# Optimization experiments

Hardware: AMD Instinct MI355X
Metric: run time of the kernel (lower is better)

Reference implementation:

```python
import jax, jax.numpy as jnp
import numpy as np

D_MODEL = 1024
N_HEADS = 16
D_HEAD = D_MODEL // N_HEADS


def setup_inputs() -> dict:
    key = jax.random.key(0)
    ks = jax.random.split(key, 16)
    B, S, D = 2, 2048, D_MODEL
    s = 1.0 / np.sqrt(D)
    inp = {
        "query": jax.random.normal(ks[0], (B, S, D), jnp.float32),
        "key": jax.random.normal(ks[1], (B, S, D), jnp.float32),
        "value": jax.random.normal(ks[2], (B, S, D), jnp.float32),
        "pos_embedding": jax.random.normal(ks[3], (B, S, D), jnp.float32),
        "Wq": jax.random.normal(ks[4], (D, D), jnp.float32) * s,
        "bq": jnp.zeros((D,), jnp.float32),
        "Wk": jax.random.normal(ks[5], (D, D), jnp.float32) * s,
        "bk": jnp.zeros((D,), jnp.float32),
        "Wv": jax.random.normal(ks[6], (D, D), jnp.float32) * s,
        "bv": jnp.zeros((D,), jnp.float32),
        "Wpos": jax.random.normal(ks[7], (D, D), jnp.float32) * s,
        "u_bias": jax.random.normal(ks[8], (N_HEADS, D_HEAD), jnp.float32) * s,
        "v_bias": jax.random.normal(ks[9], (N_HEADS, D_HEAD), jnp.float32) * s,
        "Wout": jax.random.normal(ks[10], (D, D), jnp.float32) * s,
        "bout": jnp.zeros((D,), jnp.float32),
    }
    return inp


def _rel_shift(pos_score):
    # Transformer-XL relative shift: pad one zero column, reshape, drop first row.
    B, H, S1, S2 = pos_score.shape
    zeros = jnp.zeros((B, H, S1, 1), pos_score.dtype)
    padded = jnp.concatenate([zeros, pos_score], axis=-1)  # [B,H,S1,S2+1]
    padded = padded.reshape(B, H, S2 + 1, S1)
    return padded[:, :, 1:].reshape(B, H, S1, S2)


def reference(query, key, value, pos_embedding, Wq, bq, Wk, bk, Wv, bv, Wpos, u_bias, v_bias, Wout, bout):
    B, S, D = query.shape
    H, dh = N_HEADS, D_HEAD
    q = (query @ Wq + bq).reshape(B, S, H, dh)            # [B,S,H,dh]
    k = (key @ Wk + bk).reshape(B, S, H, dh)              # [B,S,H,dh]
    v = (value @ Wv + bv).reshape(B, S, H, dh)            # [B,S,H,dh]
    p = (pos_embedding @ Wpos).reshape(B, S, H, dh)       # [B,S,H,dh]

    content_score = jnp.einsum('bqhd,bkhd->bhqk', q + u_bias, k)
    pos_score = jnp.einsum('bqhd,bkhd->bhqk', q + v_bias, p)
    pos_score = _rel_shift(pos_score)

    score = (content_score + pos_score) / jnp.asarray(np.sqrt(D), score_dtype := content_score.dtype)
    attn = jax.nn.softmax(score, axis=-1)                 # [B,H,S,S]
    context = jnp.einsum('bhqk,bkhd->bqhd', attn, v).reshape(B, S, D)
    out = context @ Wout + bout
    return out, attn
```

## Files before the change

### kernel.cpp

```cpp
#include <hip/hip_runtime.h>

#define S_LEN 2048
#define DM    1024
#define NH    16
#define DH    64
#define BATCH 2
#define S2    ((size_t)S_LEN * S_LEN)

typedef _Float16 half_t;
typedef _Float16 f16x8 __attribute__((ext_vector_type(8)));
typedef _Float16 f16x4 __attribute__((ext_vector_type(4)));
typedef float    f32x4 __attribute__((ext_vector_type(4)));

__device__ __forceinline__ void gll16(const void* g, void* l) {
  __builtin_amdgcn_global_load_lds(
      (const __attribute__((address_space(1))) void*)g,
      (__attribute__((address_space(3))) void*)l, 16, 0, 0);
}

__device__ __forceinline__ void stage_gll(half_t* lds, const half_t* src, int stride) {
  const int t = threadIdx.x, w = t >> 6, lane = t & 63;
  const int c1 = lane & 7, r8 = lane >> 3;
#pragma unroll
  for (int it = 0; it < 4; ++it) {
    int r = w * 32 + it * 8 + r8;
    const half_t* g = src + (size_t)r * stride + ((c1 ^ r8) << 3);
    gll16(g, lds + (size_t)w * 2048 + it * 512);
  }
}

__device__ __forceinline__ void mfma_block(const half_t* At, const half_t* Bt,
                                           int w, int lane, f32x4 acc[2][8]) {
  const int grp = lane >> 4, li = lane & 15;
#pragma unroll
  for (int ks = 0; ks < 2; ++ks) {
    const int chunk = ks * 4 + grp;
    f16x8 a[2], b[8];
#pragma unroll
    for (int fr = 0; fr < 2; ++fr) {
      int r = w * 32 + fr * 16 + li;
      a[fr] = *(const f16x8*)&At[(size_t)(r * 8 + (chunk ^ (r & 7))) * 8];
    }
#pragma unroll
    for (int fc = 0; fc < 8; ++fc) {
      int r = fc * 16 + li;
      b[fc] = *(const f16x8*)&Bt[(size_t)(r * 8 + (chunk ^ (r & 7))) * 8];
    }
#pragma unroll
    for (int fr = 0; fr < 2; ++fr)
#pragma unroll
      for (int fc = 0; fc < 8; ++fc)
        acc[fr][fc] = __builtin_amdgcn_mfma_f32_16x16x32_f16(a[fr], b[fc], acc[fr][fc], 0, 0, 0);
  }
}

template<typename ST>
__device__ __forceinline__ void load8s(const ST* p, float* o) {
  if constexpr (sizeof(ST) == 2) {
    f16x8 v = *(const f16x8*)p;
#pragma unroll
    for (int e = 0; e < 8; ++e) o[e] = (float)v[e];
  } else {
    const float4* q = (const float4*)p;
    float4 a = q[0], b = q[1];
    o[0]=a.x; o[1]=a.y; o[2]=a.z; o[3]=a.w; o[4]=b.x; o[5]=b.y; o[6]=b.z; o[7]=b.w;
  }
}

struct AArgs { const float* src[4]; half_t* dst[4]; };

__global__ __launch_bounds__(256) void a2h(AArgs a, half_t* zbuf) {
  if (blockIdx.x == 0 && blockIdx.y == 0 && threadIdx.x < 8) {
    float4 z = {0.f, 0.f, 0.f, 0.f};
    ((float4*)zbuf)[threadIdx.x] = z;
  }
  const float* s = a.src[blockIdx.y];
  half_t* d = a.dst[blockIdx.y];
  size_t i = ((size_t)blockIdx.x * 256 + threadIdx.x) * 8;
  float4 v0 = *(const float4*)(s + i), v1 = *(const float4*)(s + i + 4);
  f16x8 h;
  h[0]=(half_t)v0.x; h[1]=(half_t)v0.y; h[2]=(half_t)v0.z; h[3]=(half_t)v0.w;
  h[4]=(half_t)v1.x; h[5]=(half_t)v1.y; h[6]=(half_t)v1.z; h[7]=(half_t)v1.w;
  *(f16x8*)(d + i) = h;
}

struct WArgs { const float* src[5]; half_t* dst[5]; };

__global__ __launch_bounds__(256) void wconv(WArgs wa) {
  __shared__ float T[64][65];
  const float* W = wa.src[blockIdx.z];
  half_t* D = wa.dst[blockIdx.z];
  const int k0 = blockIdx.x * 64, n0 = blockIdx.y * 64;
  const int t = threadIdx.x;
#pragma unroll
  for (int it = 0; it < 4; ++it) {
    int idx = t + it * 256; int r = idx >> 4, c4 = (idx & 15) * 4;
    float4 v = *(const float4*)(W + (size_t)(k0 + r) * DM + n0 + c4);
    T[r][c4] = v.x; T[r][c4 + 1] = v.y; T[r][c4 + 2] = v.z; T[r][c4 + 3] = v.w;
  }
  __syncthreads();
#pragma unroll
  for (int it = 0; it < 2; ++it) {
    int idx = t + it * 256; int n = idx >> 3, kc = (idx & 7) * 8;
    f16x8 o;
#pragma unroll
    for (int e = 0; e < 8; ++e) o[e] = (half_t)T[kc + e][n];
    *(f16x8*)&D[(size_t)(n0 + n) * DM + k0 + kc] = o;
  }
}

struct GArgs {
  const half_t* A[4];  const half_t* Bt[4];
  const float* ba[4]; const float* bu[4]; const float* bv[4];
  half_t* oa[4]; half_t* ob[4]; float* of[4];
};

template<bool F32OUT>
__global__ __launch_bounds__(256) void gemm_k(GArgs g, int K) {
  __shared__ __align__(16) half_t At[2][128 * 64];
  __shared__ __align__(16) half_t Bt[2][128 * 64];
  const int z = blockIdx.z;
  const half_t* A = g.A[z];
  const half_t* B = g.Bt[z];
  const int n0 = blockIdx.x * 128, m0 = blockIdx.y * 128;
  const int t = threadIdx.x, w = t >> 6, lane = t & 63;
  const f32x4 zf = {0.f, 0.f, 0.f, 0.f};
  f32x4 acc[2][8];
#pragma unroll
  for (int i = 0; i < 2; ++i)
#pragma unroll
    for (int j = 0; j < 8; ++j) acc[i][j] = zf;

  stage_gll(At[0], A + (size_t)m0 * K, K);
  stage_gll(Bt[0], B + (size_t)n0 * K, K);
  __syncthreads();
  int cur = 0;
  for (int k0 = 0; k0 < K; k0 += 64) {
    int nk = k0 + 64;
    if (nk < K) {
      stage_gll(At[cur ^ 1], A + (size_t)m0 * K + nk, K);
      stage_gll(Bt[cur ^ 1], B + (size_t)n0 * K + nk, K);
    }
    mfma_block(At[cur], Bt[cur], w, lane, acc);
    __syncthreads();
    cur ^= 1;
  }
  const int grp = lane >> 4, li = lane & 15;
#pragma unroll
  for (int fr = 0; fr < 2; ++fr)
#pragma unroll
    for (int fc = 0; fc < 8; ++fc)
#pragma unroll
      for (int r = 0; r < 4; ++r) {
        int row = m0 + w * 32 + fr * 16 + grp * 4 + r;
        int col = n0 + fc * 16 + li;
        float v = acc[fr][fc][r];
        if (g.ba[z]) v += g.ba[z][col];
        if constexpr (F32OUT) {
          g.of[z][(size_t)row * DM + col] = v;
        } else {
          float v1 = v + (g.bu[z] ? g.bu[z][col] : 0.f);
          g.oa[z][(size_t)row * DM + col] = (half_t)v1;
          if (g.ob[z]) g.ob[z][(size_t)row * DM + col] = (half_t)(v + g.bv[z][col]);
        }
      }
}

__global__ __launch_bounds__(256) void vtrans(const half_t* vp, half_t* vT) {
  __shared__ half_t T[64][72];
  const int s0 = blockIdx.x * 64, h = blockIdx.y, b = blockIdx.z;
  const int t = threadIdx.x;
#pragma unroll
  for (int it = 0; it < 2; ++it) {
    int idx = t + it * 256; int s = idx >> 3, c = idx & 7;
    uint4 v = *(const uint4*)(vp + ((size_t)(b * S_LEN + s0 + s)) * DM + h * DH + c * 8);
    *(uint4*)&T[s][c * 8] = v;
  }
  __syncthreads();
  half_t* dst = vT + ((size_t)(b * NH + h)) * DH * S_LEN;
#pragma unroll
  for (int it = 0; it < 2; ++it) {
    int idx = t + it * 256; int d = idx >> 3, sc = (idx & 7) * 8;
    f16x8 o;
#pragma unroll
    for (int e = 0; e < 8; ++e) o[e] = T[sc + e][d];
    *(f16x8*)&dst[(size_t)d * S_LEN + s0 + sc] = o;
  }
}

template<typename ST>
__global__ __launch_bounds__(512) void score_fused(
    const half_t* __restrict__ qu_, const half_t* __restrict__ qv_,
    const half_t* __restrict__ kp_, const half_t* __restrict__ pp_,
    const half_t* __restrict__ zbuf, ST* __restrict__ sc, float* __restrict__ part)
{
  __shared__ __align__(16) half_t Mf[36864];
  __shared__ __align__(16) half_t QV[144 * 64];
  __shared__ __align__(16) half_t Pb[256 * 64];
  half_t* QU = Mf;
  half_t* Kt = Mf + 8192;

  const int bh = blockIdx.z, b = bh >> 4, h = bh & 15;
  const int kt = blockIdx.x, qt = blockIdx.y;
  const int i0 = qt * 128, k0 = kt * 128;
  const int base = 1920 + k0 - i0;
  const int t = threadIdx.x, w = t >> 6, lane = t & 63;
  const int grp = lane >> 4, li = lane & 15;

  {
    const half_t* srcA = qu_ + ((size_t)(b * S_LEN + i0)) * DM + h * DH;
    const half_t* srcB = kp_ + ((size_t)(b * S_LEN + k0)) * DM + h * DH;
#pragma unroll
    for (int p = 0; p < 2; ++p) {
      int cidx = t + p * 512; int r = cidx >> 3, c = cidx & 7;
      gll16(srcA + (size_t)r * DM + ((c ^ (r & 7)) << 3), QU + (size_t)cidx * 8);
      gll16(srcB + (size_t)r * DM + ((c ^ (r & 7)) << 3), Kt + (size_t)cidx * 8);
    }
  }
#pragma unroll
  for (int p = 0; p < 3; ++p) {
    int cidx = t + p * 512;
    if (cidx < 1152) {
      int r = cidx >> 3, c = cidx & 7;
      int grow = i0 + r; if (grow > S_LEN - 1) grow = S_LEN - 1;
      gll16(qv_ + ((size_t)(b * S_LEN + grow)) * DM + h * DH + ((c ^ (r & 7)) << 3),
            QV + (size_t)cidx * 8);
    }
  }
#pragma unroll
  for (int p = 0; p < 4; ++p) {
    int cidx = t + p * 512; int e = cidx >> 3, c = cidx & 7;
    int jv = base + e; if (jv >= S_LEN + 1) jv -= (S_LEN + 1);
    const half_t* src = (jv == S_LEN)
        ? (zbuf + ((c ^ (e & 7)) << 3))
        : (pp_ + ((size_t)(b * S_LEN + jv)) * DM + h * DH + ((c ^ (e & 7)) << 3));
    gll16(src, Pb + (size_t)cidx * 8);
  }
  __syncthreads();

  const f32x4 zf = {0.f, 0.f, 0.f, 0.f};
  f32x4 acc_c[8];
#pragma unroll
  for (int j = 0; j < 8; ++j) acc_c[j] = zf;
#pragma unroll
  for (int kk = 0; kk < 2; ++kk) {
    const int chunk = kk * 4 + grp;
    int ra = w * 16 + li;
    f16x8 a = *(const f16x8*)&QU[(size_t)(ra * 8 + (chunk ^ (ra & 7))) * 8];
#pragma unroll
    for (int fc = 0; fc < 8; ++fc) {
      int rb = fc * 16 + li;
      f16x8 bf = *(const f16x8*)&Kt[(size_t)(rb * 8 + (chunk ^ (rb & 7))) * 8];
      acc_c[fc] = __builtin_amdgcn_mfma_f32_16x16x32_f16(a, bf, acc_c[fc], 0, 0, 0);
    }
  }
  __syncthreads();

  f16x8 bm[2][2];
#pragma unroll
  for (int kk = 0; kk < 2; ++kk)
#pragma unroll
    for (int eci = 0; eci < 2; ++eci) {
      int rb = (w + eci * 8) * 16 + li;
      bm[kk][eci] = *(const f16x8*)&Pb[(size_t)(rb * 8 + ((kk * 4 + grp) ^ (rb & 7))) * 8];
    }
  for (int rf = 0; rf < 9; ++rf) {
    f32x4 am[2] = {zf, zf};
#pragma unroll
    for (int kk = 0; kk < 2; ++kk) {
      int ra = rf * 16 + li;
      f16x8 a = *(const f16x8*)&QV[(size_t)(ra * 8 + ((kk * 4 + grp) ^ (ra & 7))) * 8];
#pragma unroll
      for (int eci = 0; eci < 2; ++eci)
        am[eci] = __builtin_amdgcn_mfma_f32_16x16x32_f16(a, bm[kk][eci], am[eci], 0, 0, 0);
    }
#pragma unroll
    for (int eci = 0; eci < 2; ++eci) {
      int ec = w + eci * 8;
      f16x4 hv;
#pragma unroll
      for (int r = 0; r < 4; ++r) hv[r] = (half_t)am[eci][r];
      *(f16x4*)&Mf[(size_t)(((ec * 9 + rf) * 4 + grp) * 64 + li * 4)] = hv;
    }
  }
  __syncthreads();

  ST* sb = sc + (size_t)bh * S2;
  float lsum[4] = {0.f, 0.f, 0.f, 0.f};
#pragma unroll
  for (int fc = 0; fc < 8; ++fc) {
#pragma unroll
    for (int rr = 0; rr < 4; ++rr) {
      int q = w * 16 + grp * 4 + rr;
      int k = fc * 16 + li;
      int e = k - q + 127;
      int jv = base + e;
      int dlt = (jv >= S_LEN + 1) ? 1 : 0;
      int rM = q + dlt;
      int ec = e >> 4, ei = e & 15, rf = rM >> 4, ri = rM & 15;
      float mval = (float)Mf[(size_t)(((ec * 9 + rf) * 4 + (ri >> 2)) * 64 + ei * 4 + (ri & 3))];
      float s = (acc_c[fc][rr] + mval) * 0.03125f;
      float ev = __expf(s);
      sb[(size_t)(i0 + q) * S_LEN + k0 + k] = (ST)ev;
      lsum[rr] += ev;
    }
  }
#pragma unroll
  for (int rr = 0; rr < 4; ++rr) {
    float v = lsum[rr];
#pragma unroll
    for (int d = 1; d < 16; d <<= 1) v += __shfl_xor(v, d);
    if (li == 0)
      part[((size_t)bh * S_LEN + i0 + w * 16 + grp * 4 + rr) * 16 + kt] = v;
  }
}

template<typename ST>
__global__ __launch_bounds__(256) void av_attn(const ST* sc, const half_t* vT, const float* part,
                                               float* attn, half_t* ctx) {
  __shared__ __align__(16) half_t Vt[2][64 * 128];
  __shared__ float Ls[128];
  const int bh = blockIdx.y, b = bh >> 4, h = bh & 15;
  const int q0 = blockIdx.x * 128;
  const int t = threadIdx.x;
  if (t < 128) {
    const float* pp = part + ((size_t)bh * S_LEN + q0 + t) * 16;
    float L = 0.f;
#pragma unroll
    for (int k = 0; k < 16; ++k) L += pp[k];
    Ls[t] = 1.f / L;
  }
  const ST* sb = sc + (size_t)bh * S2;
  float* ab = attn + (size_t)bh * S2;
  const half_t* vb = vT + (size_t)bh * (DH * S_LEN);
  const int w = t >> 6, lane = t & 63, grp = lane >> 4, li = lane & 15;
  const int c1 = lane & 15, d4 = lane >> 4;
  const f32x4 zf = {0.f, 0.f, 0.f, 0.f};
  f32x4 acc[2][4];
#pragma unroll
  for (int i = 0; i < 2; ++i)
#pragma unroll
    for (int j = 0; j < 4; ++j) acc[i][j] = zf;

#pragma unroll
  for (int it = 0; it < 4; ++it) {
    int d = w * 16 + it * 4 + d4;
    gll16(vb + (size_t)d * S_LEN + ((c1 ^ (d & 15)) << 3), Vt[0] + (size_t)w * 2048 + it * 512);
  }
  __syncthreads();
  int cur = 0;

  for (int kt = 0; kt < 16; ++kt) {
    if (kt + 1 < 16) {
#pragma unroll
      for (int it = 0; it < 4; ++it) {
        int d = w * 16 + it * 4 + d4;
        gll16(vb + (size_t)d * S_LEN + (kt + 1) * 128 + ((c1 ^ (d & 15)) << 3),
              Vt[cur ^ 1] + (size_t)w * 2048 + it * 512);
      }
    }
#pragma unroll
    for (int ks = 0; ks < 4; ++ks) {
      f16x8 pa[2];
#pragma unroll
      for (int fr = 0; fr < 2; ++fr) {
        int r128 = w * 32 + fr * 16 + li;
        int row = q0 + r128;
        int col = kt * 128 + ks * 32 + grp * 8;
        float sv[8];
        load8s(&sb[(size_t)row * S_LEN + col], sv);
        float rL = Ls[r128];
#pragma unroll
        for (int e = 0; e < 8; ++e) sv[e] *= rL;
        float4* dst = (float4*)&ab[(size_t)row * S_LEN + col];
        float4 w0 = {sv[0], sv[1], sv[2], sv[3]};
        float4 w1 = {sv[4], sv[5], sv[6], sv[7]};
        dst[0] = w0; dst[1] = w1;
        f16x8 ph;
#pragma unroll
        for (int e = 0; e < 8; ++e) ph[e] = (half_t)sv[e];
        pa[fr] = ph;
      }
      f16x8 bf[4];
#pragma unroll
      for (int fc = 0; fc < 4; ++fc) {
        int d = fc * 16 + li; int chunk = ks * 4 + grp;
        bf[fc] = *(const f16x8*)&Vt[cur][(size_t)(d * 16 + (chunk ^ (d & 15))) * 8];
      }
#pragma unroll
      for (int fr = 0; fr < 2; ++fr)
#pragma unroll
        for (int fc = 0; fc < 4; ++fc)
          acc[fr][fc] = __builtin_amdgcn_mfma_f32_16x16x32_f16(pa[fr], bf[fc], acc[fr][fc], 0, 0, 0);
    }
    __syncthreads();
    cur ^= 1;
  }
#pragma unroll
  for (int fr = 0; fr < 2; ++fr)
#pragma unroll
    for (int fc = 0; fc < 4; ++fc)
#pragma unroll
      for (int r = 0; r < 4; ++r) {
        int q = q0 + w * 32 + fr * 16 + grp * 4 + r;
        int d = fc * 16 + li;
        ctx[((size_t)(b * S_LEN + q)) * DM + h * DH + d] = (half_t)acc[fr][fc][r];
      }
}

extern "C" void kernel_launch(void* const* d_in, const int* in_sizes, int n_in,
                              void* d_out, int out_size, void* d_ws, size_t ws_size,
                              hipStream_t stream) {
  (void)in_sizes; (void)n_in; (void)out_size;

  const float* query  = (const float*)d_in[0];
  const float* key    = (const float*)d_in[1];
  const float* value  = (const float*)d_in[2];
  const float* pos    = (const float*)d_in[3];
  const float* Wq     = (const float*)d_in[4];
  const float* bq     = (const float*)d_in[5];
  const float* Wk     = (const float*)d_in[6];
  const float* bk     = (const float*)d_in[7];
  const float* Wv     = (const float*)d_in[8];
  const float* bv     = (const float*)d_in[9];
  const float* Wpos   = (const float*)d_in[10];
  const float* u_bias = (const float*)d_in[11];
  const float* v_bias = (const float*)d_in[12];
  const float* bout   = (const float*)d_in[14];
  const float* Wout   = (const float*)d_in[13];

  float* out  = (float*)d_out;
  float* attn = out + (size_t)BATCH * S_LEN * DM;

  char* ws = (char*)d_ws;
  half_t* Wt   = (half_t*)(ws);
  half_t* Af16 = (half_t*)(ws + 10485760);
  float*  part = (float*)(ws + 10485760);
  half_t* qu   = (half_t*)(ws + 44040192);
  half_t* qv   = (half_t*)(ws + 52428800);
  half_t* kp   = (half_t*)(ws + 60817408);
  half_t* pp   = (half_t*)(ws + 69206016);
  half_t* vp   = (half_t*)(ws + 77594624);
  half_t* vT   = (half_t*)(ws + 85983232);
  half_t* ctx  = (half_t*)(ws + 77594624);
  half_t* zbuf = (half_t*)(ws + 94371840);
  half_t* scH  = (half_t*)(ws + 94375936);
  const bool fast = ws_size >= (size_t)94375936 + (size_t)BATCH * NH * S2 * 2;

  dim3 blk(256);

  AArgs aa;
  aa.src[0] = query; aa.src[1] = key; aa.src[2] = value; aa.src[3] = pos;
  for (int i = 0; i < 4; ++i) aa.dst[i] = Af16 + (size_t)i * BATCH * S_LEN * DM;
  a2h<<<dim3(2048, 4), blk, 0, stream>>>(aa, zbuf);

  WArgs wa;
  wa.src[0] = Wq; wa.src[1] = Wk; wa.src[2] = Wv; wa.src[3] = Wpos; wa.src[4] = Wout;
  for (int i = 0; i < 5; ++i) wa.dst[i] = Wt + (size_t)i * DM * DM;
  wconv<<<dim3(16, 16, 5), blk, 0, stream>>>(wa);

  GArgs ga{};
  for (int i = 0; i < 4; ++i) {
    ga.A[i]  = Af16 + (size_t)i * BATCH * S_LEN * DM;
    ga.Bt[i] = Wt + (size_t)i * DM * DM;
  }
  ga.ba[0] = bq; ga.ba[1] = bk; ga.ba[2] = bv; ga.ba[3] = nullptr;
  ga.bu[0] = u_bias; ga.bv[0] = v_bias;
  ga.oa[0] = qu; ga.oa[1] = kp; ga.oa[2] = vp; ga.oa[3] = pp;
  ga.ob[0] = qv;
  gemm_k<false><<<dim3(8, 32, 4), blk, 0, stream>>>(ga, DM);

  vtrans<<<dim3(32, 16, 2), blk, 0, stream>>>(vp, vT);

  dim3 g_sc(16, 16, 32);
  dim3 blk5(512);
  if (fast) {
    score_fused<half_t><<<g_sc, blk5, 0, stream>>>(qu, qv, kp, pp, zbuf, scH, part);
    av_attn<half_t><<<dim3(16, 32), blk, 0, stream>>>(scH, vT, part, attn, ctx);
  } else {
    float* scF = attn;
    score_fused<float><<<g_sc, blk5, 0, stream>>>(qu, qv, kp, pp, zbuf, scF, part);
    av_attn<float><<<dim3(16, 32), blk, 0, stream>>>(scF, vT, part, attn, ctx);
  }

  GArgs go{};
  go.A[0] = ctx; go.Bt[0] = Wt + (size_t)4 * DM * DM;
  go.ba[0] = bout; go.of[0] = out;
  gemm_k<true><<<dim3(8, 32, 1), blk, 0, stream>>>(go, DM);
}
```

Measured before the change: 585.8 us.

## Shrink score kernel LDS footprint by aliasing buffers and special-casing the extra row

Cuts the score kernel's shared memory from about 123KB to 80KB. The QU, Kt and Pb staging buffers now alias one region that is reused for the M matrix, and the QV tile shrinks from 144 to 128 rows. The extra 129th row needed by the relative shift is computed from registers with a single MFMA and stored in an unused slot of M. Launch bounds request 4 waves per SIMD, so two blocks can fit per CU to improve latency hiding, at the cost of extra branches in the epilogue and tighter register limits.

```diff
diff --git a/kernel.cpp b/kernel.cpp
--- a/kernel.cpp
+++ b/kernel.cpp
@@ -189,16 +189,17 @@
 }
 
 template<typename ST>
-__global__ __launch_bounds__(512) void score_fused(
+__global__ __launch_bounds__(512, 4) void score_fused(
     const half_t* __restrict__ qu_, const half_t* __restrict__ qv_,
     const half_t* __restrict__ kp_, const half_t* __restrict__ pp_,
     const half_t* __restrict__ zbuf, ST* __restrict__ sc, float* __restrict__ part)
 {
-  __shared__ __align__(16) half_t Mf[36864];
-  __shared__ __align__(16) half_t QV[144 * 64];
-  __shared__ __align__(16) half_t Pb[256 * 64];
-  half_t* QU = Mf;
-  half_t* Kt = Mf + 8192;
+  __shared__ __align__(16) half_t RegA[32768];
+  __shared__ __align__(16) half_t QV[128 * 64];
+  half_t* QU = RegA;
+  half_t* Kt = RegA + 8192;
+  half_t* Pb = RegA + 16384;
+  half_t* Mf = RegA;
 
   const int bh = blockIdx.z, b = bh >> 4, h = bh & 15;
   const int kt = blockIdx.x, qt = blockIdx.y;
@@ -210,21 +211,14 @@
   {
     const half_t* srcA = qu_ + ((size_t)(b * S_LEN + i0)) * DM + h * DH;
     const half_t* srcB = kp_ + ((size_t)(b * S_LEN + k0)) * DM + h * DH;
+    const half_t* srcQ = qv_ + ((size_t)(b * S_LEN + i0)) * DM + h * DH;
 #pragma unroll
     for (int p = 0; p < 2; ++p) {
       int cidx = t + p * 512; int r = cidx >> 3, c = cidx & 7;
-      gll16(srcA + (size_t)r * DM + ((c ^ (r & 7)) << 3), QU + (size_t)cidx * 8);
-      gll16(srcB + (size_t)r * DM + ((c ^ (r & 7)) << 3), Kt + (size_t)cidx * 8);
-    }
-  }
-#pragma unroll
-  for (int p = 0; p < 3; ++p) {
-    int cidx = t + p * 512;
-    if (cidx < 1152) {
-      int r = cidx >> 3, c = cidx & 7;
-      int grow = i0 + r; if (grow > S_LEN - 1) grow = S_LEN - 1;
-      gll16(qv_ + ((size_t)(b * S_LEN + grow)) * DM + h * DH + ((c ^ (r & 7)) << 3),
-            QV + (size_t)cidx * 8);
+      size_t off = (size_t)r * DM + ((c ^ (r & 7)) << 3);
+      gll16(srcA + off, QU + (size_t)cidx * 8);
+      gll16(srcB + off, Kt + (size_t)cidx * 8);
+      gll16(srcQ + off, QV + (size_t)cidx * 8);
     }
   }
 #pragma unroll
@@ -236,6 +230,14 @@
         : (pp_ + ((size_t)(b * S_LEN + jv)) * DM + h * DH + ((c ^ (e & 7)) << 3));
     gll16(src, Pb + (size_t)cidx * 8);
   }
+
+  f16x8 aq[2];
+  {
+    int r128 = i0 + 128; if (r128 > S_LEN - 1) r128 = S_LEN - 1;
+    const half_t* q128p = qv_ + ((size_t)(b * S_LEN + r128)) * DM + h * DH;
+    aq[0] = *(const f16x8*)(q128p + (0 * 4 + grp) * 8);
+    aq[1] = *(const f16x8*)(q128p + (1 * 4 + grp) * 8);
+  }
   __syncthreads();
 
   const f32x4 zf = {0.f, 0.f, 0.f, 0.f};
@@ -254,8 +256,6 @@
       acc_c[fc] = __builtin_amdgcn_mfma_f32_16x16x32_f16(a, bf, acc_c[fc], 0, 0, 0);
     }
   }
-  __syncthreads();
-
   f16x8 bm[2][2];
 #pragma unroll
   for (int kk = 0; kk < 2; ++kk)
@@ -264,7 +264,9 @@
       int rb = (w + eci * 8) * 16 + li;
       bm[kk][eci] = *(const f16x8*)&Pb[(size_t)(rb * 8 + ((kk * 4 + grp) ^ (rb & 7))) * 8];
     }
-  for (int rf = 0; rf < 9; ++rf) {
+  __syncthreads();
+
+  for (int rf = 0; rf < 8; ++rf) {
     f32x4 am[2] = {zf, zf};
 #pragma unroll
     for (int kk = 0; kk < 2; ++kk) {
@@ -277,10 +279,23 @@
 #pragma unroll
     for (int eci = 0; eci < 2; ++eci) {
       int ec = w + eci * 8;
-      f16x4 hv;
-#pragma unroll
-      for (int r = 0; r < 4; ++r) hv[r] = (half_t)am[eci][r];
-      *(f16x4*)&Mf[(size_t)(((ec * 9 + rf) * 4 + grp) * 64 + li * 4)] = hv;
+      if (!(ec == 15 && li == 15)) {
+        f16x4 hv;
+#pragma unroll
+        for (int r = 0; r < 4; ++r) hv[r] = (half_t)am[eci][r];
+        *(f16x4*)&Mf[(size_t)(((ec * 8 + rf) * 4 + grp) * 64 + li * 4)] = hv;
+      }
+    }
+  }
+
+  {
+    f32x4 am0 = zf;
+#pragma unroll
+    for (int kk = 0; kk < 2; ++kk)
+      am0 = __builtin_amdgcn_mfma_f32_16x16x32_f16(aq[kk], bm[kk][0], am0, 0, 0, 0);
+    if (grp == 0) {
+      int e = w * 16 + li;
+      Mf[(size_t)(((120 + (e >> 4)) * 4 + ((e >> 2) & 3)) * 64 + 60 + (e & 3))] = (half_t)am0[0];
     }
   }
   __syncthreads();
@@ -297,8 +312,13 @@
       int jv = base + e;
       int dlt = (jv >= S_LEN + 1) ? 1 : 0;
       int rM = q + dlt;
-      int ec = e >> 4, ei = e & 15, rf = rM >> 4, ri = rM & 15;
-      float mval = (float)Mf[(size_t)(((ec * 9 + rf) * 4 + (ri >> 2)) * 64 + ei * 4 + (ri & 3))];
+      float mval;
+      if (rM < 128) {
+        int ec = e >> 4, ei = e & 15, rf = rM >> 4, ri = rM & 15;
+        mval = (float)Mf[(size_t)(((ec * 8 + rf) * 4 + (ri >> 2)) * 64 + ei * 4 + (ri & 3))];
+      } else {
+        mval = (float)Mf[(size_t)(((120 + (e >> 4)) * 4 + ((e >> 2) & 3)) * 64 + 60 + (e & 3))];
+      }
       float s = (acc_c[fc][rr] + mval) * 0.03125f;
       float ev = __expf(s);
       sb[(size_t)(i0 + q) * S_LEN + k0 + k] = (ST)ev;
@@ -426,8 +446,8 @@
   const float* Wpos   = (const float*)d_in[10];
   const float* u_bias = (const float*)d_in[11];
   const float* v_bias = (const float*)d_in[12];
+  const float* Wout   = (const float*)d_in[13];
   const float* bout   = (const float*)d_in[14];
-  const float* Wout   = (const float*)d_in[13];
 
   float* out  = (float*)d_out;
   float* attn = out + (size_t)BATCH * S_LEN * DM;
```

New measurement: 542.7 us. 7.3% less time.
